# Performance work log

Measured on AMD Instinct MI355X. Metric: run time of the kernel, lower is better.

The kernel has to match this reference:

```python
import jax, jax.numpy as jnp
import numpy as np

H = 1024          # hidden_size
V = 32000         # output_size (vocab)
B = 32            # batch
T = 64            # MAX_SEQ_LENGTH
SOS = 0           # SOS_token


def setup_inputs() -> dict:
    key = jax.random.key(0)
    ks = jax.random.split(key, 9)
    s = 1.0 / np.sqrt(H)
    return {
        "encoder_outputs": jax.random.normal(ks[0], (B, 48, H), jnp.float32),
        "encoder_hidden": jax.random.normal(ks[1], (1, B, H), jnp.float32),
        "emb": jax.random.normal(ks[2], (V, H), jnp.float32) * 0.02,
        "W_ih": jax.random.uniform(ks[3], (3 * H, H), jnp.float32, -s, s),
        "W_hh": jax.random.uniform(ks[4], (3 * H, H), jnp.float32, -s, s),
        "b_ih": jax.random.uniform(ks[5], (3 * H,), jnp.float32, -s, s),
        "b_hh": jax.random.uniform(ks[6], (3 * H,), jnp.float32, -s, s),
        "W_out": jax.random.uniform(ks[7], (V, H), jnp.float32, -s, s),
        "b_out": jax.random.uniform(ks[8], (V,), jnp.float32, -s, s),
    }


def _gru_cell(x, h, W_ih, W_hh, b_ih, b_hh):
    # PyTorch GRU cell math
    gi = x @ W_ih.T + b_ih                      # [B, 3H]
    gh = h @ W_hh.T + b_hh                      # [B, 3H]
    i_r, i_z, i_n = jnp.split(gi, 3, axis=-1)
    h_r, h_z, h_n = jnp.split(gh, 3, axis=-1)
    r = jax.nn.sigmoid(i_r + h_r)
    z = jax.nn.sigmoid(i_z + h_z)
    n = jnp.tanh(i_n + r * h_n)
    return (1.0 - z) * n + z * h


def reference(encoder_outputs, encoder_hidden, emb, W_ih, W_hh, b_ih, b_hh, W_out, b_out):
    batch = encoder_outputs.shape[0]
    h0 = encoder_hidden[0]                      # decoder_hidden = encoder_hidden[:num_layers], [B, H]
    tok0 = jnp.full((batch,), SOS, dtype=jnp.int32)

    def step(carry, _):
        h, tok = carry
        x = jax.nn.relu(emb[tok])               # embedding + relu, [B, H]
        h_new = _gru_cell(x, h, W_ih, W_hh, b_ih, b_hh)
        logits = h_new @ W_out.T + b_out        # [B, V]
        tok_new = jnp.argmax(logits, axis=-1).astype(jnp.int32)  # greedy topk(1)
        return (h_new, tok_new), logits

    (hT, _), logits = jax.lax.scan(step, (h0, tok0), None, length=T)
    logits = jnp.transpose(logits, (1, 0, 2))   # [B, T, V]
    log_probs = jax.nn.log_softmax(logits, axis=-1)
    return log_probs, hT[None]                  # decoder_hidden shape [num_layers, B, H]
```

## Files before the change

### kernel.cpp

```cpp
#include <hip/hip_runtime.h>
#include <stdint.h>

namespace {

constexpr int H = 1024;
constexpr int V = 32000;
constexpr int B = 32;
constexpr int T = 64;
constexpr int NPART = V / 64;
constexpr long long OUT_LOGITS = (long long)B * T * V;

__device__ __forceinline__ uint32_t ord_f32(float f) {
    uint32_t u = __float_as_uint(f);
    return (u & 0x80000000u) ? ~u : (u | 0x80000000u);
}
__device__ __forceinline__ uint64_t pack_key(float val, int idx) {
    return ((uint64_t)ord_f32(val) << 32) | (uint64_t)(0xFFFFFFFFu - (uint32_t)idx);
}
__device__ __forceinline__ int key_idx(uint64_t k) {
    return (int)(0xFFFFFFFFu - (uint32_t)k);
}
__device__ __forceinline__ uint64_t shfl_xor_u64(uint64_t x, int mask) {
    int lo = __shfl_xor((int)(uint32_t)x, mask);
    int hi = __shfl_xor((int)(uint32_t)(x >> 32), mask);
    return ((uint64_t)(uint32_t)hi << 32) | (uint32_t)lo;
}
__device__ __forceinline__ uint64_t umax64(uint64_t a, uint64_t b) { return a > b ? a : b; }
__device__ __forceinline__ float sigmoidf_(float x) { return 1.0f / (1.0f + expf(-x)); }

__device__ __forceinline__ const float* uniform_ptr(const float* p) {
    uintptr_t a = (uintptr_t)p;
    uint32_t lo = (uint32_t)__builtin_amdgcn_readfirstlane((int)(uint32_t)a);
    uint32_t hi = (uint32_t)__builtin_amdgcn_readfirstlane((int)(uint32_t)(a >> 32));
    return (const float*)(((uintptr_t)hi << 32) | lo);
}

__global__ __launch_bounds__(256)
void transpose_kernel(const float* __restrict__ src, float* __restrict__ dst) {
    __shared__ float tile[32][33];
    int vt = blockIdx.x * 32;
    int kt = blockIdx.y * 32;
    int tx = threadIdx.x & 31, ty = threadIdx.x >> 5;
#pragma unroll
    for (int i = 0; i < 32; i += 8)
        tile[ty + i][tx] = src[(size_t)(vt + ty + i) * H + kt + tx];
    __syncthreads();
#pragma unroll
    for (int i = 0; i < 32; i += 8)
        dst[(size_t)(kt + ty + i) * V + vt + tx] = tile[tx][ty + i];
}

__global__ __launch_bounds__(1024)
void gru_kernel(const float* __restrict__ h_prev,
                const float* __restrict__ emb,
                const float* __restrict__ W_ih,
                const float* __restrict__ W_hh,
                const float* __restrict__ b_ih,
                const float* __restrict__ b_hh,
                const uint64_t* __restrict__ amax,
                int use_tok,
                float* __restrict__ h_new,
                float* __restrict__ h_newT)
{
    int j = blockIdx.x;
    int wave = threadIdx.x >> 6;
    int lane = threadIdx.x & 63;
    int b0 = wave * 2, b1 = wave * 2 + 1;

    int tok0 = 0, tok1 = 0;
    if (use_tok) {
        uint64_t k0 = 0, k1 = 0;
        for (int i = lane; i < NPART; i += 64) {
            k0 = umax64(k0, amax[b0 * NPART + i]);
            k1 = umax64(k1, amax[b1 * NPART + i]);
        }
#pragma unroll
        for (int d = 32; d; d >>= 1) {
            k0 = umax64(k0, shfl_xor_u64(k0, d));
            k1 = umax64(k1, shfl_xor_u64(k1, d));
        }
        tok0 = key_idx(k0);
        tok1 = key_idx(k1);
    }

    const float2* x0_2  = (const float2*)(emb + (size_t)tok0 * H);
    const float2* x1_2  = (const float2*)(emb + (size_t)tok1 * H);
    const float* hp0 = h_prev + (size_t)b0 * H;
    const float* hp1 = h_prev + (size_t)b1 * H;
    const float2* hp0_2 = (const float2*)hp0;
    const float2* hp1_2 = (const float2*)hp1;
    const float* wr = W_ih + (size_t)j * H;
    const float2* wr2 = (const float2*)wr;
    const float2* wz2 = (const float2*)(wr + (size_t)H * H);
    const float2* wn2 = (const float2*)(wr + (size_t)2 * H * H);
    const float* ur = W_hh + (size_t)j * H;
    const float2* ur2 = (const float2*)ur;
    const float2* uz2 = (const float2*)(ur + (size_t)H * H);
    const float2* un2 = (const float2*)(ur + (size_t)2 * H * H);

    float a[12];
#pragma unroll
    for (int i = 0; i < 12; ++i) a[i] = 0.f;

#pragma unroll 1
    for (int i = 0; i < 8; ++i) {
        int f = lane + i * 64;
        float2 xv0 = x0_2[f], xv1 = x1_2[f];
        float2 hv0 = hp0_2[f], hv1 = hp1_2[f];
        float2 w1 = wr2[f], w2 = wz2[f], w3 = wn2[f];
        float2 u1 = ur2[f], u2 = uz2[f], u3 = un2[f];
        xv0.x = fmaxf(xv0.x, 0.f); xv0.y = fmaxf(xv0.y, 0.f);
        xv1.x = fmaxf(xv1.x, 0.f); xv1.y = fmaxf(xv1.y, 0.f);
        a[0]  = fmaf(w1.x, xv0.x, fmaf(w1.y, xv0.y, a[0]));
        a[1]  = fmaf(w2.x, xv0.x, fmaf(w2.y, xv0.y, a[1]));
        a[2]  = fmaf(w3.x, xv0.x, fmaf(w3.y, xv0.y, a[2]));
        a[3]  = fmaf(u1.x, hv0.x, fmaf(u1.y, hv0.y, a[3]));
        a[4]  = fmaf(u2.x, hv0.x, fmaf(u2.y, hv0.y, a[4]));
        a[5]  = fmaf(u3.x, hv0.x, fmaf(u3.y, hv0.y, a[5]));
        a[6]  = fmaf(w1.x, xv1.x, fmaf(w1.y, xv1.y, a[6]));
        a[7]  = fmaf(w2.x, xv1.x, fmaf(w2.y, xv1.y, a[7]));
        a[8]  = fmaf(w3.x, xv1.x, fmaf(w3.y, xv1.y, a[8]));
        a[9]  = fmaf(u1.x, hv1.x, fmaf(u1.y, hv1.y, a[9]));
        a[10] = fmaf(u2.x, hv1.x, fmaf(u2.y, hv1.y, a[10]));
        a[11] = fmaf(u3.x, hv1.x, fmaf(u3.y, hv1.y, a[11]));
    }
#pragma unroll
    for (int i = 0; i < 12; ++i) {
#pragma unroll
        for (int d = 32; d; d >>= 1) a[i] += __shfl_xor(a[i], d);
    }

    if (lane == 0) {
        float bir = b_ih[j], biz = b_ih[j + H], bin = b_ih[j + 2 * H];
        float bhr = b_hh[j], bhz = b_hh[j + H], bhn = b_hh[j + 2 * H];
        {
            float r = sigmoidf_((a[0] + bir) + (a[3] + bhr));
            float z = sigmoidf_((a[1] + biz) + (a[4] + bhz));
            float n = tanhf((a[2] + bin) + r * (a[5] + bhn));
            float o = (1.f - z) * n + z * hp0[j];
            h_new[(size_t)b0 * H + j] = o;
            h_newT[(size_t)j * B + b0] = o;
        }
        {
            float r = sigmoidf_((a[6] + bir) + (a[9] + bhr));
            float z = sigmoidf_((a[7] + biz) + (a[10] + bhz));
            float n = tanhf((a[8] + bin) + r * (a[11] + bhn));
            float o = (1.f - z) * n + z * hp1[j];
            h_new[(size_t)b1 * H + j] = o;
            h_newT[(size_t)j * B + b1] = o;
        }
    }
}

__global__ __launch_bounds__(512, 4)
void logits_mm_kernel(const float* __restrict__ WT,
                      const float* __restrict__ hT,
                      float* __restrict__ out,
                      float* __restrict__ part1,
                      int t)
{
    const int bid  = blockIdx.x;
    const int vt   = bid >> 1;
    const int kh   = bid & 1;
    const int wave = threadIdx.x >> 6;
    const int lane = threadIdx.x & 63;
    const int k0   = kh * 512 + wave * 64;
    const int v    = vt * 128 + lane * 2;

    const float* wp = WT + (size_t)k0 * V + v;
    const float* hrow = uniform_ptr(hT + (size_t)k0 * B);

    float acc[32][2];
#pragma unroll
    for (int b = 0; b < 32; ++b) { acc[b][0] = 0.f; acc[b][1] = 0.f; }

    float2 wcur = *(const float2*)wp;
    wp += V;

#pragma unroll 1
    for (int k = 0; k < 64; ++k) {
        float2 wnxt = *(const float2*)wp;
        wp += V;
        const float4* h4 = (const float4*)hrow;
        hrow += B;
#pragma unroll
        for (int q = 0; q < 8; ++q) {
            float4 hv = h4[q];
            acc[4 * q + 0][0] = fmaf(hv.x, wcur.x, acc[4 * q + 0][0]);
            acc[4 * q + 0][1] = fmaf(hv.x, wcur.y, acc[4 * q + 0][1]);
            acc[4 * q + 1][0] = fmaf(hv.y, wcur.x, acc[4 * q + 1][0]);
            acc[4 * q + 1][1] = fmaf(hv.y, wcur.y, acc[4 * q + 1][1]);
            acc[4 * q + 2][0] = fmaf(hv.z, wcur.x, acc[4 * q + 2][0]);
            acc[4 * q + 2][1] = fmaf(hv.z, wcur.y, acc[4 * q + 2][1]);
            acc[4 * q + 3][0] = fmaf(hv.w, wcur.x, acc[4 * q + 3][0]);
            acc[4 * q + 3][1] = fmaf(hv.w, wcur.y, acc[4 * q + 3][1]);
        }
        wcur = wnxt;
    }

    __shared__ float red[8][2048];
#pragma unroll
    for (int bg = 0; bg < 2; ++bg) {
#pragma unroll
        for (int bl = 0; bl < 16; ++bl) {
            int bb = bg * 16 + bl;
            *(float2*)&red[wave][bl * 128 + lane * 2] = make_float2(acc[bb][0], acc[bb][1]);
        }
        __syncthreads();
#pragma unroll
        for (int q = 0; q < 4; ++q) {
            int c = threadIdx.x + q * 512;
            float s = red[0][c];
#pragma unroll
            for (int w = 1; w < 8; ++w) s += red[w][c];
            int bl = c >> 7, vloc = c & 127;
            int b = bg * 16 + bl;
            int vv = vt * 128 + vloc;
            if (kh == 0) out[((size_t)b * T + t) * V + vv] = s;
            else         part1[(size_t)b * V + vv] = s;
        }
        __syncthreads();
    }
}

__global__ __launch_bounds__(512)
void combine_kernel(float* __restrict__ out,
                    const float* __restrict__ part1,
                    const float* __restrict__ b_out,
                    int t,
                    uint64_t* __restrict__ amax)
{
    const int vt   = blockIdx.x;
    const int wave = threadIdx.x >> 6;
    const int lane = threadIdx.x & 63;
    const int v    = vt * 64 + lane;
    const float bias = b_out[v];
#pragma unroll
    for (int bi = 0; bi < 4; ++bi) {
        int b = wave * 4 + bi;
        size_t o = ((size_t)b * T + t) * V + v;
        float s = out[o] + part1[(size_t)b * V + v] + bias;
        out[o] = s;
        uint64_t key = pack_key(s, v);
#pragma unroll
        for (int d = 32; d; d >>= 1) key = umax64(key, shfl_xor_u64(key, d));
        if (lane == 0) amax[(size_t)b * NPART + vt] = key;
    }
}

__global__ __launch_bounds__(256)
void logsoftmax_kernel(float* __restrict__ out) {
    size_t row = (size_t)blockIdx.x * V;
    int lane = threadIdx.x & 63, wave = threadIdx.x >> 6;
    __shared__ float red[4];

    float m = -INFINITY;
    for (int v = threadIdx.x; v < V; v += 256) m = fmaxf(m, out[row + v]);
#pragma unroll
    for (int d = 32; d; d >>= 1) m = fmaxf(m, __shfl_xor(m, d));
    if (lane == 0) red[wave] = m;
    __syncthreads();
    float M = fmaxf(fmaxf(red[0], red[1]), fmaxf(red[2], red[3]));
    __syncthreads();

    float s = 0.f;
    for (int v = threadIdx.x; v < V; v += 256) s += expf(out[row + v] - M);
#pragma unroll
    for (int d = 32; d; d >>= 1) s += __shfl_xor(s, d);
    if (lane == 0) red[wave] = s;
    __syncthreads();
    float S = red[0] + red[1] + red[2] + red[3];

    float L = M + logf(S);
    for (int v = threadIdx.x; v < V; v += 256) out[row + v] -= L;
}

__global__ __launch_bounds__(256)
void copy_h_kernel(const float* __restrict__ h, float* __restrict__ out) {
    int i = blockIdx.x * 256 + threadIdx.x;
    out[OUT_LOGITS + i] = h[i];
}

}

extern "C" void kernel_launch(void* const* d_in, const int* in_sizes, int n_in,
                              void* d_out, int out_size, void* d_ws, size_t ws_size,
                              hipStream_t stream) {
    const float* enc_hidden = (const float*)d_in[1];
    const float* emb   = (const float*)d_in[2];
    const float* W_ih  = (const float*)d_in[3];
    const float* W_hh  = (const float*)d_in[4];
    const float* b_ih  = (const float*)d_in[5];
    const float* b_hh  = (const float*)d_in[6];
    const float* W_out = (const float*)d_in[7];
    const float* b_out = (const float*)d_in[8];
    float* out = (float*)d_out;

    float* ws = (float*)d_ws;
    const size_t WT_FLOATS = (size_t)V * H;
    float* WT    = ws;
    float* part1 = ws + WT_FLOATS;
    float* hA    = part1 + (size_t)B * V;
    float* hB    = hA + 32768;
    float* hTA   = hB + 32768;
    float* hTB   = hTA + 32768;
    uint64_t* amax = (uint64_t*)(hTB + 32768);

    transpose_kernel<<<dim3(1000, 32), 256, 0, stream>>>(W_out, WT);

    for (int t = 0; t < T; ++t) {
        const float* hp = (t == 0) ? enc_hidden : ((t & 1) ? hA : hB);
        float* hn  = (t & 1) ? hB : hA;
        float* hnT = (t & 1) ? hTB : hTA;
        gru_kernel<<<H, 1024, 0, stream>>>(hp, emb, W_ih, W_hh, b_ih, b_hh,
                                           amax, t == 0 ? 0 : 1, hn, hnT);
        logits_mm_kernel<<<500, 512, 0, stream>>>(WT, hnT, out, part1, t);
        combine_kernel<<<500, 512, 0, stream>>>(out, part1, b_out, t, amax);
    }

    logsoftmax_kernel<<<B * T, 256, 0, stream>>>(out);
    copy_h_kernel<<<32768 / 256, 256, 0, stream>>>(hB, out);
}
```

Baseline: 8.896 ms.

## Fuse logits split-K partials, bias, and argmax into single 1024-thread kernel

Replaces the two-way split-K logits matmul plus separate combine kernel with one kernel per 128-column vocab tile that reduces all 16 K-slices in shared memory, adds bias, writes logits and the per-tile argmax key. This removes a kernel launch per step and the write and read of the part1 partial buffer plus the re-read of out. It also deepens the weight prefetch to four loads in flight. It halves the grid to 250 blocks of 1024 threads, which may under-occupy the GPU, and the amax partition count changes to V/128, which the GRU kernel's reader must match.

Measured after the change: 8.413 ms. 1.06x faster.

```diff
diff --git a/kernel.cpp b/kernel.cpp
--- a/kernel.cpp
+++ b/kernel.cpp
@@ -7,7 +7,7 @@
 constexpr int V = 32000;
 constexpr int B = 32;
 constexpr int T = 64;
-constexpr int NPART = V / 64;
+constexpr int NPART = V / 128;
 constexpr long long OUT_LOGITS = (long long)B * T * V;
 
 __device__ __forceinline__ uint32_t ord_f32(float f) {
@@ -152,19 +152,18 @@
     }
 }
 
-__global__ __launch_bounds__(512, 4)
-void logits_mm_kernel(const float* __restrict__ WT,
-                      const float* __restrict__ hT,
-                      float* __restrict__ out,
-                      float* __restrict__ part1,
-                      int t)
+__global__ __launch_bounds__(1024, 4)
+void logits_full_kernel(const float* __restrict__ WT,
+                        const float* __restrict__ hT,
+                        const float* __restrict__ b_out,
+                        float* __restrict__ out,
+                        int t,
+                        uint64_t* __restrict__ amax)
 {
-    const int bid  = blockIdx.x;
-    const int vt   = bid >> 1;
-    const int kh   = bid & 1;
+    const int vt   = blockIdx.x;
     const int wave = threadIdx.x >> 6;
     const int lane = threadIdx.x & 63;
-    const int k0   = kh * 512 + wave * 64;
+    const int k0   = wave * 64;
     const int v    = vt * 128 + lane * 2;
 
     const float* wp = WT + (size_t)k0 * V + v;
@@ -174,11 +173,12 @@
 #pragma unroll
     for (int b = 0; b < 32; ++b) { acc[b][0] = 0.f; acc[b][1] = 0.f; }
 
-    float2 wcur = *(const float2*)wp;
-    wp += V;
-
-#pragma unroll 1
-    for (int k = 0; k < 64; ++k) {
+    float2 w0 = *(const float2*)wp; wp += V;
+    float2 w1 = *(const float2*)wp; wp += V;
+    float2 w2 = *(const float2*)wp; wp += V;
+    float2 w3 = *(const float2*)wp; wp += V;
+
+    auto wstep = [&](float2& wreg) {
         float2 wnxt = *(const float2*)wp;
         wp += V;
         const float4* h4 = (const float4*)hrow;
@@ -186,65 +186,53 @@
 #pragma unroll
         for (int q = 0; q < 8; ++q) {
             float4 hv = h4[q];
-            acc[4 * q + 0][0] = fmaf(hv.x, wcur.x, acc[4 * q + 0][0]);
-            acc[4 * q + 0][1] = fmaf(hv.x, wcur.y, acc[4 * q + 0][1]);
-            acc[4 * q + 1][0] = fmaf(hv.y, wcur.x, acc[4 * q + 1][0]);
-            acc[4 * q + 1][1] = fmaf(hv.y, wcur.y, acc[4 * q + 1][1]);
-            acc[4 * q + 2][0] = fmaf(hv.z, wcur.x, acc[4 * q + 2][0]);
-            acc[4 * q + 2][1] = fmaf(hv.z, wcur.y, acc[4 * q + 2][1]);
-            acc[4 * q + 3][0] = fmaf(hv.w, wcur.x, acc[4 * q + 3][0]);
-            acc[4 * q + 3][1] = fmaf(hv.w, wcur.y, acc[4 * q + 3][1]);
-        }
-        wcur = wnxt;
-    }
-
-    __shared__ float red[8][2048];
-#pragma unroll
-    for (int bg = 0; bg < 2; ++bg) {
-#pragma unroll
-        for (int bl = 0; bl < 16; ++bl) {
-            int bb = bg * 16 + bl;
+            acc[4 * q + 0][0] = fmaf(hv.x, wreg.x, acc[4 * q + 0][0]);
+            acc[4 * q + 0][1] = fmaf(hv.x, wreg.y, acc[4 * q + 0][1]);
+            acc[4 * q + 1][0] = fmaf(hv.y, wreg.x, acc[4 * q + 1][0]);
+            acc[4 * q + 1][1] = fmaf(hv.y, wreg.y, acc[4 * q + 1][1]);
+            acc[4 * q + 2][0] = fmaf(hv.z, wreg.x, acc[4 * q + 2][0]);
+            acc[4 * q + 2][1] = fmaf(hv.z, wreg.y, acc[4 * q + 2][1]);
+            acc[4 * q + 3][0] = fmaf(hv.w, wreg.x, acc[4 * q + 3][0]);
+            acc[4 * q + 3][1] = fmaf(hv.w, wreg.y, acc[4 * q + 3][1]);
+        }
+        wreg = wnxt;
+    };
+
+#pragma unroll 1
+    for (int k = 0; k < 64; k += 4) {
+        wstep(w0);
+        wstep(w1);
+        wstep(w2);
+        wstep(w3);
+    }
+
+    __shared__ float red[16][1024];
+#pragma unroll
+    for (int bg = 0; bg < 4; ++bg) {
+#pragma unroll
+        for (int bl = 0; bl < 8; ++bl) {
+            int bb = bg * 8 + bl;
             *(float2*)&red[wave][bl * 128 + lane * 2] = make_float2(acc[bb][0], acc[bb][1]);
         }
         __syncthreads();
-#pragma unroll
-        for (int q = 0; q < 4; ++q) {
-            int c = threadIdx.x + q * 512;
-            float s = red[0][c];
-#pragma unroll
-            for (int w = 1; w < 8; ++w) s += red[w][c];
-            int bl = c >> 7, vloc = c & 127;
-            int b = bg * 16 + bl;
-            int vv = vt * 128 + vloc;
-            if (kh == 0) out[((size_t)b * T + t) * V + vv] = s;
-            else         part1[(size_t)b * V + vv] = s;
+        if (wave < 8) {
+            int b = bg * 8 + wave;
+            float s0 = 0.f, s1 = 0.f;
+#pragma unroll
+            for (int kw = 0; kw < 16; ++kw) {
+                float2 r = *(const float2*)&red[kw][wave * 128 + lane * 2];
+                s0 += r.x; s1 += r.y;
+            }
+            float2 bias = *(const float2*)&b_out[v];
+            s0 += bias.x; s1 += bias.y;
+            *(float2*)&out[((size_t)b * T + t) * V + v] = make_float2(s0, s1);
+
+            uint64_t key = umax64(pack_key(s0, v), pack_key(s1, v + 1));
+#pragma unroll
+            for (int d = 32; d; d >>= 1) key = umax64(key, shfl_xor_u64(key, d));
+            if (lane == 0) amax[(size_t)b * NPART + vt] = key;
         }
         __syncthreads();
-    }
-}
-
-__global__ __launch_bounds__(512)
-void combine_kernel(float* __restrict__ out,
-                    const float* __restrict__ part1,
-                    const float* __restrict__ b_out,
-                    int t,
-                    uint64_t* __restrict__ amax)
-{
-    const int vt   = blockIdx.x;
-    const int wave = threadIdx.x >> 6;
-    const int lane = threadIdx.x & 63;
-    const int v    = vt * 64 + lane;
-    const float bias = b_out[v];
-#pragma unroll
-    for (int bi = 0; bi < 4; ++bi) {
-        int b = wave * 4 + bi;
-        size_t o = ((size_t)b * T + t) * V + v;
-        float s = out[o] + part1[(size_t)b * V + v] + bias;
-        out[o] = s;
-        uint64_t key = pack_key(s, v);
-#pragma unroll
-        for (int d = 32; d; d >>= 1) key = umax64(key, shfl_xor_u64(key, d));
-        if (lane == 0) amax[(size_t)b * NPART + vt] = key;
     }
 }
 
@@ -299,8 +287,7 @@
     float* ws = (float*)d_ws;
     const size_t WT_FLOATS = (size_t)V * H;
     float* WT    = ws;
-    float* part1 = ws + WT_FLOATS;
-    float* hA    = part1 + (size_t)B * V;
+    float* hA    = ws + WT_FLOATS;
     float* hB    = hA + 32768;
     float* hTA   = hB + 32768;
     float* hTB   = hTA + 32768;
@@ -314,8 +301,7 @@
         float* hnT = (t & 1) ? hTB : hTA;
         gru_kernel<<<H, 1024, 0, stream>>>(hp, emb, W_ih, W_hh, b_ih, b_hh,
                                            amax, t == 0 ? 0 : 1, hn, hnT);
-        logits_mm_kernel<<<500, 512, 0, stream>>>(WT, hnT, out, part1, t);
-        combine_kernel<<<500, 512, 0, stream>>>(out, part1, b_out, t, amax);
+        logits_full_kernel<<<V / 128, 1024, 0, stream>>>(WT, hnT, b_out, out, t, amax);
     }
 
     logsoftmax_kernel<<<B * T, 256, 0, stream>>>(out);
```
